# Kernel optimization log

Hardware: AMD Instinct MI355X
Metric: run time of the kernel (lower is better)

The kernel has to match this reference:

```python
import jax, jax.numpy as jnp
import numpy as np

B, N, A, D = 16, 256, 64, 256


def setup_inputs() -> dict:
    key = jax.random.key(0)
    ks = jax.random.split(key, 9)
    s = 1.0 / np.sqrt(D)
    return {
        "cc_embeds": jax.random.normal(ks[0], (B, N, D), jnp.float32),
        "anchor_embeds": jax.random.normal(ks[1], (B, N, A, D), jnp.float32),
        "sims": jax.random.normal(ks[2], (B, N, A), jnp.float32),
        "Wq": jax.random.normal(ks[3], (D, D), jnp.float32) * s,
        "bq": jax.random.normal(ks[4], (D,), jnp.float32) * s,
        "Wk": jax.random.normal(ks[5], (D, D), jnp.float32) * s,
        "bk": jax.random.normal(ks[6], (D,), jnp.float32) * s,
        "Wv": jax.random.normal(ks[7], (D, D), jnp.float32) * s,
        "bv": jax.random.normal(ks[8], (D,), jnp.float32) * s,
    }


def reference(cc_embeds, anchor_embeds, sims, Wq, bq, Wk, bk, Wv, bv):
    # Linear projections (torch nn.Linear: x @ W.T + b)
    Q = cc_embeds @ Wq.T + bq                    # [B, N, D]
    K = anchor_embeds @ Wk.T + bk                # [B, N, A, D]
    V = anchor_embeds @ Wv.T + bv                # [B, N, A, D]
    scale = 1.0 / jnp.sqrt(jnp.asarray(D, Q.dtype))
    scores = jnp.einsum('bnd,bnad->bna', Q, K) * scale  # [B, N, A]
    adj = scores + sims                          # additive similarity bias
    # conditional softmax: rows whose raw sum == 0 are passed through unchanged
    nonzero = jnp.sum(adj, axis=-1, keepdims=True) != 0
    probs = jnp.where(nonzero, jax.nn.softmax(adj, axis=-1), adj)
    out = jnp.einsum('bna,bnad->bnd', probs, V)  # [B, N, D]
    return out[:, :, None, :]                    # match torch output [B, N, 1, D]
```

## Files before the change

kernel.cpp:

```cpp
#include <hip/hip_runtime.h>
#include <hip/hip_bf16.h>


#define AS 257

__global__ __launch_bounds__(256) void k1_prep(
    const float* __restrict__ Wq, const float* __restrict__ bq,
    const float* __restrict__ Wk, const float* __restrict__ bk,
    const float* __restrict__ Wv,
    float* __restrict__ M, float* __restrict__ rvec, float* __restrict__ uvec,
    float* __restrict__ s0, float* __restrict__ WvT) {
  __shared__ float colL[256];
  __shared__ float pr[256];
  __shared__ float tile[64][65];
  const int tid = threadIdx.x;
  const int bid = blockIdx.x;
  if (bid < 256) {
    colL[tid] = Wq[tid * 256 + bid];
    __syncthreads();
    float acc = 0.f;
#pragma unroll 4
    for (int d = 0; d < 256; ++d) acc += colL[d] * Wk[d * 256 + tid];
    M[bid * 256 + tid] = acc;
  } else if (bid == 256) {
    colL[tid] = bq[tid];
    __syncthreads();
    float acc = 0.f;
#pragma unroll 4
    for (int d = 0; d < 256; ++d) acc += colL[d] * Wk[d * 256 + tid];
    rvec[tid] = acc;
  } else if (bid == 257) {
    colL[tid] = bk[tid];
    pr[tid] = bq[tid] * bk[tid];
    __syncthreads();
    float acc = 0.f;
#pragma unroll 4
    for (int d = 0; d < 256; ++d) acc += Wq[d * 256 + tid] * colL[d];
    uvec[tid] = acc;
    if (tid == 0) {
      float s = 0.f;
      for (int d = 0; d < 256; ++d) s += pr[d];
      s0[0] = s;
    }
  } else {
    const int tb = bid - 258, bi = tb >> 2, bj = tb & 3;
#pragma unroll
    for (int k = 0; k < 16; ++k) {
      int idx = k * 256 + tid;
      int r = idx >> 6, cL = idx & 63;
      tile[r][cL] = Wv[(bi * 64 + r) * 256 + bj * 64 + cL];
    }
    __syncthreads();
#pragma unroll
    for (int k = 0; k < 16; ++k) {
      int idx = k * 256 + tid;
      int r = idx >> 6, cL = idx & 63;
      WvT[(bj * 64 + r) * 256 + bi * 64 + cL] = tile[cL][r];
    }
  }
}

__global__ __launch_bounds__(256) void k2_proj(
    const float* __restrict__ cc, const float* __restrict__ M,
    const float* __restrict__ rvec, const float* __restrict__ uvec,
    const float* __restrict__ s0p,
    float* __restrict__ tmat, float* __restrict__ cvec) {
  __shared__ float ccT[256 * 12];
  __shared__ float uL[256];
  const int tid = threadIdx.x;
  const int i0 = blockIdx.x * 8;
  const float4* g4 = (const float4*)(cc + (size_t)i0 * 256);
#pragma unroll
  for (int k = 0; k < 2; ++k) {
    int f = k * 256 + tid;
    float4 v = g4[f];
    int row = f >> 6;
    int e = (f & 63) << 2;
    ccT[(e + 0) * 12 + row] = v.x;
    ccT[(e + 1) * 12 + row] = v.y;
    ccT[(e + 2) * 12 + row] = v.z;
    ccT[(e + 3) * 12 + row] = v.w;
  }
  uL[tid] = uvec[tid];
  __syncthreads();
  float acc[8] = {0.f, 0.f, 0.f, 0.f, 0.f, 0.f, 0.f, 0.f};
#pragma unroll 4
  for (int e = 0; e < 256; ++e) {
    float m = M[e * 256 + tid];
    const float* crow = &ccT[e * 12];
#pragma unroll
    for (int r = 0; r < 8; ++r) acc[r] += crow[r] * m;
  }
  float rv = rvec[tid];
#pragma unroll
  for (int r = 0; r < 8; ++r) tmat[(size_t)(i0 + r) * 256 + tid] = acc[r] + rv;
  const int r = tid >> 5, j = tid & 31;
  float pc = 0.f;
#pragma unroll
  for (int k = 0; k < 8; ++k) pc += ccT[(j + 32 * k) * 12 + r] * uL[j + 32 * k];
  for (int off = 16; off >= 1; off >>= 1) pc += __shfl_xor(pc, off, 32);
  if (j == 0) cvec[i0 + r] = pc + s0p[0];
}

__global__ __launch_bounds__(256) void k3_attn(
    const float* __restrict__ anchor, const float* __restrict__ sims,
    const float* __restrict__ tmat, const float* __restrict__ cvec,
    float* __restrict__ wout, float* __restrict__ psum) {
  __shared__ float aL[64 * AS];
  __shared__ float tL[256];
  __shared__ float partial[4][64];
  __shared__ float probsL[64];
  __shared__ float psh;
  const int i = blockIdx.x;
  const int tid = threadIdx.x;
  const float4* g4 = (const float4*)(anchor + (size_t)i * 16384);
#pragma unroll
  for (int k = 0; k < 16; ++k) {
    int f = k * 256 + tid;
    float4 v = g4[f];
    int row = f >> 6;
    int c4 = (f & 63) << 2;
    float* dst = &aL[row * AS + c4];
    dst[0] = v.x; dst[1] = v.y; dst[2] = v.z; dst[3] = v.w;
  }
  tL[tid] = tmat[(size_t)i * 256 + tid];
  __syncthreads();
  const int lane = tid & 63, w = tid >> 6;
  {
    const float* a0 = &aL[lane * AS + w * 64];
    const float* t0 = &tL[w * 64];
    float s = 0.f;
#pragma unroll
    for (int j = 0; j < 64; ++j) s += a0[j] * t0[j];
    partial[w][lane] = s;
  }
  __syncthreads();
  if (tid < 64) {
    float adj = partial[0][tid] + partial[1][tid] + partial[2][tid] + partial[3][tid];
    adj = (adj + cvec[i]) * 0.0625f + sims[(size_t)i * 64 + tid];
    float ssum = adj, smax = adj;
    for (int off = 32; off >= 1; off >>= 1) {
      ssum += __shfl_xor(ssum, off, 64);
      smax = fmaxf(smax, __shfl_xor(smax, off, 64));
    }
    float p;
    if (ssum != 0.f) {
      p = expf(adj - smax);
      float z = p;
      for (int off = 32; off >= 1; off >>= 1) z += __shfl_xor(z, off, 64);
      p = p / z;
    } else {
      p = adj;
    }
    float ps = p;
    for (int off = 32; off >= 1; off >>= 1) ps += __shfl_xor(ps, off, 64);
    probsL[tid] = p;
    if (tid == 0) psh = ps;
  }
  __syncthreads();
  float acc = 0.f;
#pragma unroll
  for (int a = 0; a < 64; ++a) acc += probsL[a] * aL[a * AS + tid];
  wout[(size_t)i * 256 + tid] = acc;
  if (tid == 0) psum[i] = psh;
}

__global__ __launch_bounds__(256) void k4_out(
    const float* __restrict__ wmat, const float* __restrict__ WvT,
    const float* __restrict__ bv, const float* __restrict__ psum,
    float* __restrict__ out) {
  __shared__ float wT[256 * 12];
  __shared__ float psL[8];
  const int tid = threadIdx.x;
  const int i0 = blockIdx.x * 8;
  const float4* g4 = (const float4*)(wmat + (size_t)i0 * 256);
#pragma unroll
  for (int k = 0; k < 2; ++k) {
    int f = k * 256 + tid;
    float4 v = g4[f];
    int row = f >> 6;
    int e = (f & 63) << 2;
    wT[(e + 0) * 12 + row] = v.x;
    wT[(e + 1) * 12 + row] = v.y;
    wT[(e + 2) * 12 + row] = v.z;
    wT[(e + 3) * 12 + row] = v.w;
  }
  if (tid < 8) psL[tid] = psum[i0 + tid];
  __syncthreads();
  float acc[8] = {0.f, 0.f, 0.f, 0.f, 0.f, 0.f, 0.f, 0.f};
#pragma unroll 4
  for (int e = 0; e < 256; ++e) {
    float m = WvT[e * 256 + tid];
    const float* wr = &wT[e * 12];
#pragma unroll
    for (int r = 0; r < 8; ++r) acc[r] += wr[r] * m;
  }
  float b = bv[tid];
#pragma unroll
  for (int r = 0; r < 8; ++r)
    out[(size_t)(i0 + r) * 256 + tid] = acc[r] + b * psL[r];
}

extern "C" void kernel_launch(void* const* d_in, const int* in_sizes, int n_in,
                              void* d_out, int out_size, void* d_ws, size_t ws_size,
                              hipStream_t stream) {
  const float* cc     = (const float*)d_in[0];
  const float* anchor = (const float*)d_in[1];
  const float* sims   = (const float*)d_in[2];
  const float* Wq     = (const float*)d_in[3];
  const float* bq     = (const float*)d_in[4];
  const float* Wk     = (const float*)d_in[5];
  const float* bk     = (const float*)d_in[6];
  const float* Wv     = (const float*)d_in[7];
  const float* bv     = (const float*)d_in[8];
  float* out = (float*)d_out;
  float* ws  = (float*)d_ws;

  float* M    = ws;
  float* WvT  = ws + 65536;
  float* rvec = ws + 131072;
  float* uvec = ws + 131328;
  float* s0   = ws + 131584;
  float* cvec = ws + 131840;
  float* psum = ws + 135936;
  float* tmat = ws + 140032;
  float* wmat = tmat + 1048576;

  k1_prep<<<274, 256, 0, stream>>>(Wq, bq, Wk, bk, Wv, M, rvec, uvec, s0, WvT);
  k2_proj<<<512, 256, 0, stream>>>(cc, M, rvec, uvec, s0, tmat, cvec);
  k3_attn<<<4096, 256, 0, stream>>>(anchor, sims, tmat, cvec, wmat, psum);
  k4_out<<<512, 256, 0, stream>>>(wmat, WvT, bv, psum, out);
}
```

Measured before the change: 461.8 us.

## Keep anchor tile in registers in attention kernel instead of shared memory

The attention kernel no longer stages each 64x256 anchor tile in a padded 64 KB shared buffer. Each thread holds 16 float4 values in registers, computes scores with wave-level shuffle reductions, and reduces the weighted sum across the four waves through a small shared array. This removes the large LDS footprint that limited occupancy and the scalar LDS traffic, at the cost of more registers per thread. The projection kernels also switch their transposed shared tiles from stride 12 to stride 8 so each row can be read as two float4 loads.

```diff
diff --git a/kernel.cpp b/kernel.cpp
--- a/kernel.cpp
+++ b/kernel.cpp
@@ -1,8 +1,6 @@
 #include <hip/hip_runtime.h>
 #include <hip/hip_bf16.h>
 
-
-#define AS 257
 
 __global__ __launch_bounds__(256) void k1_prep(
     const float* __restrict__ Wq, const float* __restrict__ bq,
@@ -65,7 +63,7 @@
     const float* __restrict__ rvec, const float* __restrict__ uvec,
     const float* __restrict__ s0p,
     float* __restrict__ tmat, float* __restrict__ cvec) {
-  __shared__ float ccT[256 * 12];
+  __shared__ __align__(16) float ccT[256 * 8];
   __shared__ float uL[256];
   const int tid = threadIdx.x;
   const int i0 = blockIdx.x * 8;
@@ -76,10 +74,10 @@
     float4 v = g4[f];
     int row = f >> 6;
     int e = (f & 63) << 2;
-    ccT[(e + 0) * 12 + row] = v.x;
-    ccT[(e + 1) * 12 + row] = v.y;
-    ccT[(e + 2) * 12 + row] = v.z;
-    ccT[(e + 3) * 12 + row] = v.w;
+    ccT[(e + 0) * 8 + row] = v.x;
+    ccT[(e + 1) * 8 + row] = v.y;
+    ccT[(e + 2) * 8 + row] = v.z;
+    ccT[(e + 3) * 8 + row] = v.w;
   }
   uL[tid] = uvec[tid];
   __syncthreads();
@@ -87,9 +85,10 @@
 #pragma unroll 4
   for (int e = 0; e < 256; ++e) {
     float m = M[e * 256 + tid];
-    const float* crow = &ccT[e * 12];
-#pragma unroll
-    for (int r = 0; r < 8; ++r) acc[r] += crow[r] * m;
+    const float4* cr = (const float4*)(ccT + e * 8);
+    float4 c0 = cr[0], c1 = cr[1];
+    acc[0] += c0.x * m; acc[1] += c0.y * m; acc[2] += c0.z * m; acc[3] += c0.w * m;
+    acc[4] += c1.x * m; acc[5] += c1.y * m; acc[6] += c1.z * m; acc[7] += c1.w * m;
   }
   float rv = rvec[tid];
 #pragma unroll
@@ -97,7 +96,7 @@
   const int r = tid >> 5, j = tid & 31;
   float pc = 0.f;
 #pragma unroll
-  for (int k = 0; k < 8; ++k) pc += ccT[(j + 32 * k) * 12 + r] * uL[j + 32 * k];
+  for (int k = 0; k < 8; ++k) pc += ccT[(j + 32 * k) * 8 + r] * uL[j + 32 * k];
   for (int off = 16; off >= 1; off >>= 1) pc += __shfl_xor(pc, off, 32);
   if (j == 0) cvec[i0 + r] = pc + s0p[0];
 }
@@ -106,38 +105,30 @@
     const float* __restrict__ anchor, const float* __restrict__ sims,
     const float* __restrict__ tmat, const float* __restrict__ cvec,
     float* __restrict__ wout, float* __restrict__ psum) {
-  __shared__ float aL[64 * AS];
-  __shared__ float tL[256];
-  __shared__ float partial[4][64];
-  __shared__ float probsL[64];
+  __shared__ float sL[64];
+  __shared__ float pL[64];
+  __shared__ __align__(16) float pW[4 * 256];
   __shared__ float psh;
   const int i = blockIdx.x;
   const int tid = threadIdx.x;
+  const int lane = tid & 63, w = tid >> 6;
+
   const float4* g4 = (const float4*)(anchor + (size_t)i * 16384);
+  float4 v[16];
+#pragma unroll
+  for (int k = 0; k < 16; ++k) v[k] = g4[k * 256 + tid];
+  const float4 t4 = ((const float4*)(tmat + (size_t)i * 256))[lane];
+
 #pragma unroll
   for (int k = 0; k < 16; ++k) {
-    int f = k * 256 + tid;
-    float4 v = g4[f];
-    int row = f >> 6;
-    int c4 = (f & 63) << 2;
-    float* dst = &aL[row * AS + c4];
-    dst[0] = v.x; dst[1] = v.y; dst[2] = v.z; dst[3] = v.w;
-  }
-  tL[tid] = tmat[(size_t)i * 256 + tid];
-  __syncthreads();
-  const int lane = tid & 63, w = tid >> 6;
-  {
-    const float* a0 = &aL[lane * AS + w * 64];
-    const float* t0 = &tL[w * 64];
-    float s = 0.f;
-#pragma unroll
-    for (int j = 0; j < 64; ++j) s += a0[j] * t0[j];
-    partial[w][lane] = s;
+    float s = v[k].x * t4.x + v[k].y * t4.y + v[k].z * t4.z + v[k].w * t4.w;
+#pragma unroll
+    for (int off = 32; off >= 1; off >>= 1) s += __shfl_xor(s, off, 64);
+    if (lane == 0) sL[k * 4 + w] = s;
   }
   __syncthreads();
   if (tid < 64) {
-    float adj = partial[0][tid] + partial[1][tid] + partial[2][tid] + partial[3][tid];
-    adj = (adj + cvec[i]) * 0.0625f + sims[(size_t)i * 64 + tid];
+    float adj = (sL[tid] + cvec[i]) * 0.0625f + sims[(size_t)i * 64 + tid];
     float ssum = adj, smax = adj;
     for (int off = 32; off >= 1; off >>= 1) {
       ssum += __shfl_xor(ssum, off, 64);
@@ -154,14 +145,21 @@
     }
     float ps = p;
     for (int off = 32; off >= 1; off >>= 1) ps += __shfl_xor(ps, off, 64);
-    probsL[tid] = p;
+    pL[tid] = p;
     if (tid == 0) psh = ps;
   }
   __syncthreads();
-  float acc = 0.f;
-#pragma unroll
-  for (int a = 0; a < 64; ++a) acc += probsL[a] * aL[a * AS + tid];
-  wout[(size_t)i * 256 + tid] = acc;
+  float4 acc = {0.f, 0.f, 0.f, 0.f};
+#pragma unroll
+  for (int k = 0; k < 16; ++k) {
+    float p = pL[k * 4 + w];
+    acc.x += p * v[k].x; acc.y += p * v[k].y;
+    acc.z += p * v[k].z; acc.w += p * v[k].w;
+  }
+  ((float4*)(pW + w * 256))[lane] = acc;
+  __syncthreads();
+  float val = pW[tid] + pW[256 + tid] + pW[512 + tid] + pW[768 + tid];
+  wout[(size_t)i * 256 + tid] = val;
   if (tid == 0) psum[i] = psh;
 }
 
@@ -169,7 +167,7 @@
     const float* __restrict__ wmat, const float* __restrict__ WvT,
     const float* __restrict__ bv, const float* __restrict__ psum,
     float* __restrict__ out) {
-  __shared__ float wT[256 * 12];
+  __shared__ __align__(16) float wT[256 * 8];
   __shared__ float psL[8];
   const int tid = threadIdx.x;
   const int i0 = blockIdx.x * 8;
@@ -180,10 +178,10 @@
     float4 v = g4[f];
     int row = f >> 6;
     int e = (f & 63) << 2;
-    wT[(e + 0) * 12 + row] = v.x;
-    wT[(e + 1) * 12 + row] = v.y;
-    wT[(e + 2) * 12 + row] = v.z;
-    wT[(e + 3) * 12 + row] = v.w;
+    wT[(e + 0) * 8 + row] = v.x;
+    wT[(e + 1) * 8 + row] = v.y;
+    wT[(e + 2) * 8 + row] = v.z;
+    wT[(e + 3) * 8 + row] = v.w;
   }
   if (tid < 8) psL[tid] = psum[i0 + tid];
   __syncthreads();
@@ -191,9 +189,10 @@
 #pragma unroll 4
   for (int e = 0; e < 256; ++e) {
     float m = WvT[e * 256 + tid];
-    const float* wr = &wT[e * 12];
-#pragma unroll
-    for (int r = 0; r < 8; ++r) acc[r] += wr[r] * m;
+    const float4* wr = (const float4*)(wT + e * 8);
+    float4 c0 = wr[0], c1 = wr[1];
+    acc[0] += c0.x * m; acc[1] += c0.y * m; acc[2] += c0.z * m; acc[3] += c0.w * m;
+    acc[4] += c1.x * m; acc[5] += c1.y * m; acc[6] += c1.z * m; acc[7] += c1.w * m;
   }
   float b = bv[tid];
 #pragma unroll
```

New measurement: 461.0 us. About the same (-0.2%).
